# Kernel optimization log

Hardware: AMD Instinct MI355X
Metric: run time of the kernel (lower is better)

Reference implementation:

```python
import jax, jax.numpy as jnp
import numpy as np
from jax import lax

DIM = 96; HEADS = 3; WS = 8; SS = 4; HRES = 256; WRES = 256
HD = DIM // HEADS; SCALE = HD ** -0.5; N = WS * WS


def _rel_pos():
    # signed-log relative coordinates, [N, N, 2]
    c = np.arange(WS)
    coords = np.stack(np.meshgrid(c, c, indexing='ij')).reshape(2, -1)
    rel = (coords[:, :, None] - coords[:, None, :]).transpose(1, 2, 0).astype(np.float32)
    return np.sign(rel) * np.log1p(np.abs(rel))


def _attn_mask():
    # Swin-style shift mask, [nW, N, N] with 0 / -100
    img = np.zeros((HRES, WRES), np.float32)
    sl = (slice(0, -WS), slice(-WS, -SS), slice(-SS, None))
    cnt = 0
    for hs in sl:
        for ws in sl:
            img[hs, ws] = cnt
            cnt += 1
    mw = img.reshape(HRES // WS, WS, WRES // WS, WS).transpose(0, 2, 1, 3).reshape(-1, N)
    d = mw[:, None, :] - mw[:, :, None]
    return np.where(d != 0, -100.0, 0.0).astype(np.float32)

REL = jnp.asarray(_rel_pos())
MASK = jnp.asarray(_attn_mask())


def _conv1x1(x, w, b):
    return jnp.einsum('oc,bchw->bohw', w, x) + b[None, :, None, None]


def setup_inputs() -> dict:
    key = jax.random.key(0)
    ks = jax.random.split(key, 14)
    f = lambda k, s, sc=0.02: jax.random.normal(k, s, jnp.float32) * sc
    return {
        'x':   jax.random.normal(ks[0], (4, DIM, HRES, WRES), jnp.float32),
        'Wv':  f(ks[1], (DIM, DIM)),       'bv':  f(ks[2], (DIM,)),
        'Wqk': f(ks[3], (2 * DIM, DIM)),   'bqk': f(ks[4], (2 * DIM,)),
        'Wm1': f(ks[5], (2, 256), 0.1),    'bm1': f(ks[6], (256,)),
        'Wm2': f(ks[7], (256, HEADS), 0.1),'bm2': f(ks[8], (HEADS,)),
        'Wdw': f(ks[9], (DIM, 1, 5, 5)),   'bdw': f(ks[10], (DIM,)),
        'Wp':  f(ks[11], (DIM, DIM)),      'bp':  f(ks[12], (DIM,)),
    }


def reference(x, Wv, bv, Wqk, bqk, Wm1, bm1, Wm2, bm2, Wdw, bdw, Wp, bp):
    B, C, H, W = x.shape
    V = _conv1x1(x, Wv, bv)                      # [B,C,H,W]
    QK = _conv1x1(x, Wqk, bqk)                   # [B,2C,H,W]
    qkv = jnp.concatenate([QK, V], axis=1).transpose(0, 2, 3, 1)  # [B,H,W,3C]
    qkv = jnp.roll(qkv, (-SS, -SS), axis=(1, 2))
    nh, nw = H // WS, W // WS
    win = qkv.reshape(B, nh, WS, nw, WS, 3 * C).transpose(0, 1, 3, 2, 4, 5)
    win = win.reshape(B * nh * nw, N, 3 * C)     # [B_, N, 3C]
    q, k, v = [t.reshape(-1, N, HEADS, HD).transpose(0, 2, 1, 3)
               for t in jnp.split(win, 3, axis=-1)]
    attn = jnp.einsum('bhnd,bhmd->bhnm', q * SCALE, k)           # [B_,h,N,N]
    bias = jax.nn.relu(REL @ Wm1 + bm1) @ Wm2 + bm2              # [N,N,h]
    attn = attn + bias.transpose(2, 0, 1)[None]
    attn = attn.reshape(B, nh * nw, HEADS, N, N) + MASK[None, :, None]
    attn = jax.nn.softmax(attn.reshape(-1, HEADS, N, N), axis=-1)
    out = jnp.einsum('bhnm,bhmd->bnhd', attn, v).reshape(-1, N, C)
    out = out.reshape(B, nh, nw, WS, WS, C).transpose(0, 1, 3, 2, 4, 5).reshape(B, H, W, C)
    out = jnp.roll(out, (SS, SS), axis=(1, 2)).transpose(0, 3, 1, 2)  # [B,C,H,W]
    Vp = jnp.pad(V, ((0, 0), (0, 0), (2, 2), (2, 2)), mode='reflect')
    conv = lax.conv_general_dilated(Vp, Wdw, (1, 1), 'VALID',
                                    feature_group_count=C,
                                    dimension_numbers=('NCHW', 'OIHW', 'NCHW'))
    conv = conv + bdw[None, :, None, None]
    return _conv1x1(conv + out, Wp, bp)
```

## Files before the change

### kernel.cpp

```cpp
#include <hip/hip_runtime.h>
#include <hip/hip_bf16.h>
#include <hip/hip_fp16.h>

#define NHEADS 3
#define SSH 4
#define NWD 32
#define PXI 65536
#define SCALE 0.17677669529663687f

__global__ __launch_bounds__(256) void k0_wt(
    const float* __restrict__ Wqk, const float* __restrict__ Wv,
    const float* __restrict__ Wp, float* __restrict__ WT,
    float* __restrict__ WTp) {
  int i = blockIdx.x * 256 + threadIdx.x;
  if (i < 288 * 96) {
    int c = i % 96, oc = i / 96;
    float w = (oc < 192) ? Wqk[oc * 96 + c] : Wv[(oc - 192) * 96 + c];
    WT[c * 288 + oc] = w;
  }
  if (i < 96 * 96) {
    int c = i % 96, oc = i / 96;
    WTp[c * 96 + oc] = Wp[oc * 96 + c];
  }
}

__global__ __launch_bounds__(256) void k1_qkv(
    const float* __restrict__ x, const float* __restrict__ WT,
    const float* __restrict__ bqk, const float* __restrict__ bv,
    __half* __restrict__ qkv_h, float* __restrict__ v_b, int b) {
  __shared__ __align__(16) float Xt[96 * 64];
  const int tid = threadIdx.x;
  const int pt = blockIdx.x, ot = blockIdx.y;
  const int p0 = pt * 64;

  for (int i = tid; i < 96 * 16; i += 256) {
    int c = i >> 4, f = i & 15;
    *(float4*)&Xt[c * 64 + f * 4] =
        *(const float4*)&x[(size_t)(b * 96 + c) * PXI + p0 + f * 4];
  }
  __syncthreads();

  const int lane = tid & 63;
  const int wvu = __builtin_amdgcn_readfirstlane(tid >> 6);
  const int oc0l = wvu * 24;
  const int oc0 = ot * 96 + oc0l;

  float acc[24];
#pragma unroll
  for (int r = 0; r < 24; r++) acc[r] = 0.f;

  const float* wt = WT + oc0;
#pragma unroll 4
  for (int c = 0; c < 96; c++) {
    float xa = Xt[c * 64 + lane];
    const float* wc = wt + c * 288;
#pragma unroll
    for (int r = 0; r < 24; r++) acc[r] += wc[r] * xa;
  }

#pragma unroll
  for (int r = 0; r < 24; r++) {
    int oc = oc0 + r;
    acc[r] += (oc < 192) ? bqk[oc] : bv[oc - 192];
  }

  {
    int p = p0 + lane;
    int h = p >> 8, w = p & 255;
    int hp = (h + 252) & 255, wp = (w + 252) & 255;
    int win = (hp >> 3) * NWD + (wp >> 3);
    int n = (hp & 7) * 8 + (wp & 7);

    __align__(16) __half2 hv[12];
#pragma unroll
    for (int r = 0; r < 12; r++)
      hv[r] = __floats2half2_rn(acc[2 * r], acc[2 * r + 1]);
    __half* dst = qkv_h + (size_t)(win * 64 + n) * 288 + oc0;
    const float4* hv4 = (const float4*)hv;
    *(float4*)&dst[0]  = hv4[0];
    *(float4*)&dst[8]  = hv4[1];
    *(float4*)&dst[16] = hv4[2];

    if (ot == 2) {
#pragma unroll
      for (int r = 0; r < 24; r++)
        v_b[(size_t)(oc0l + r) * PXI + p] = acc[r];
    }
  }
}

__global__ __launch_bounds__(256) void k2_bias(
    const float* __restrict__ Wm1, const float* __restrict__ bm1,
    const float* __restrict__ Wm2, const float* __restrict__ bm2,
    float* __restrict__ bias_ws) {
  int pair = blockIdx.x * 256 + threadIdx.x;
  int n = pair >> 6, m = pair & 63;
  float d0 = (float)((n >> 3) - (m >> 3));
  float d1 = (float)((n & 7) - (m & 7));
  float r0 = (d0 > 0.f ? 1.f : (d0 < 0.f ? -1.f : 0.f)) * log1pf(fabsf(d0));
  float r1 = (d1 > 0.f ? 1.f : (d1 < 0.f ? -1.f : 0.f)) * log1pf(fabsf(d1));
  float a0 = 0.f, a1 = 0.f, a2 = 0.f;
  for (int j = 0; j < 256; j++) {
    float hb = r0 * Wm1[j] + r1 * Wm1[256 + j] + bm1[j];
    hb = fmaxf(hb, 0.f);
    a0 += hb * Wm2[j * 3 + 0];
    a1 += hb * Wm2[j * 3 + 1];
    a2 += hb * Wm2[j * 3 + 2];
  }
  bias_ws[0 * 4096 + pair] = a0 + bm2[0];
  bias_ws[1 * 4096 + pair] = a1 + bm2[1];
  bias_ws[2 * 4096 + pair] = a2 + bm2[2];
}

__global__ __launch_bounds__(64, 4) void k3_attn(
    const __half* __restrict__ qkv_h, const float* __restrict__ bias_ws,
    float* __restrict__ o_b) {
  __shared__ __align__(16) float KV[64 * 36];
  const int lane = threadIdx.x;
  const int win = blockIdx.x;
  const int hd = blockIdx.y;
  const int wh = win >> 5, ww = win & 31;
  const int row8 = lane >> 3, c4 = (lane & 7) * 4;

  const __half* qrow = qkv_h + (size_t)(win * 64 + lane) * 288 + hd * 32;
  float4 qraw[4];
  const float4* qp = (const float4*)qrow;
#pragma unroll
  for (int t = 0; t < 4; t++) qraw[t] = qp[t];

  const __half* kbase = qkv_h + (size_t)win * 64 * 288 + 96 + hd * 32;
  float2 kraw[8];
#pragma unroll
  for (int t = 0; t < 8; t++)
    kraw[t] = *(const float2*)&kbase[(size_t)(t * 8 + row8) * 288 + c4];

#pragma unroll
  for (int t = 0; t < 8; t++) {
    const __half2* hh = (const __half2*)&kraw[t];
    float2 a = __half22float2(hh[0]), b2 = __half22float2(hh[1]);
    *(float4*)&KV[(t * 8 + row8) * 36 + c4] = make_float4(a.x, a.y, b2.x, b2.y);
  }

  float q[32];
#pragma unroll
  for (int t = 0; t < 4; t++) {
    const __half2* hh = (const __half2*)&qraw[t];
#pragma unroll
    for (int u = 0; u < 4; u++) {
      float2 f = __half22float2(hh[u]);
      q[8 * t + 2 * u + 0] = f.x * SCALE;
      q[8 * t + 2 * u + 1] = f.y * SCALE;
    }
  }

  const float* bw = bias_ws + hd * 4096 + lane * 64;
  float s[64];
#pragma unroll
  for (int t = 0; t < 16; t++) {
    float4 b4 = *(const float4*)&bw[4 * t];
    s[4 * t + 0] = b4.x; s[4 * t + 1] = b4.y;
    s[4 * t + 2] = b4.z; s[4 * t + 3] = b4.w;
  }

  if (wh == 31 || ww == 31) {
    int rn = ((wh == 31) ? ((row8 < 4) ? 1 : 2) : 0) * 3 +
             ((ww == 31) ? (((lane & 7) < 4) ? 1 : 2) : 0);
#pragma unroll
    for (int m = 0; m < 64; m++) {
      int rm = ((wh == 31) ? (((m >> 3) < 4) ? 1 : 2) : 0) * 3 +
               ((ww == 31) ? (((m & 7) < 4) ? 1 : 2) : 0);
      if (rm != rn) s[m] -= 100.f;
    }
  }

#pragma unroll
  for (int m = 0; m < 64; m++) {
    float sum = s[m];
#pragma unroll
    for (int t = 0; t < 8; t++) {
      float4 kk = *(const float4*)&KV[m * 36 + 4 * t];
      sum += q[4 * t + 0] * kk.x + q[4 * t + 1] * kk.y +
             q[4 * t + 2] * kk.z + q[4 * t + 3] * kk.w;
    }
    s[m] = sum;
  }

  float2 vraw[8];
#pragma unroll
  for (int t = 0; t < 8; t++)
    vraw[t] = *(const float2*)&kbase[(size_t)(t * 8 + row8) * 288 + 96 + c4];

  float tr[32];
#pragma unroll
  for (int i = 0; i < 32; i++) tr[i] = fmaxf(s[i], s[i + 32]);
#pragma unroll
  for (int i = 0; i < 16; i++) tr[i] = fmaxf(tr[i], tr[i + 16]);
#pragma unroll
  for (int i = 0; i < 8; i++) tr[i] = fmaxf(tr[i], tr[i + 8]);
#pragma unroll
  for (int i = 0; i < 4; i++) tr[i] = fmaxf(tr[i], tr[i + 4]);
  float mx = fmaxf(fmaxf(tr[0], tr[1]), fmaxf(tr[2], tr[3]));
#pragma unroll
  for (int m = 0; m < 64; m++) s[m] = __expf(s[m] - mx);
#pragma unroll
  for (int i = 0; i < 32; i++) tr[i] = s[i] + s[i + 32];
#pragma unroll
  for (int i = 0; i < 16; i++) tr[i] = tr[i] + tr[i + 16];
#pragma unroll
  for (int i = 0; i < 8; i++) tr[i] = tr[i] + tr[i + 8];
#pragma unroll
  for (int i = 0; i < 4; i++) tr[i] = tr[i] + tr[i + 4];
  float inv = 1.f / ((tr[0] + tr[1]) + (tr[2] + tr[3]));

#pragma unroll
  for (int t = 0; t < 8; t++) {
    const __half2* hh = (const __half2*)&vraw[t];
    float2 a = __half22float2(hh[0]), b2 = __half22float2(hh[1]);
    *(float4*)&KV[(t * 8 + row8) * 36 + c4] = make_float4(a.x, a.y, b2.x, b2.y);
  }

  float o[32];
#pragma unroll
  for (int d = 0; d < 32; d++) o[d] = 0.f;
#pragma unroll
  for (int m = 0; m < 64; m++) {
    float p = s[m];
#pragma unroll
    for (int t = 0; t < 8; t++) {
      float4 vv = *(const float4*)&KV[m * 36 + 4 * t];
      o[4 * t + 0] += p * vv.x;
      o[4 * t + 1] += p * vv.y;
      o[4 * t + 2] += p * vv.z;
      o[4 * t + 3] += p * vv.w;
    }
  }

  const int hpix = ((wh << 3) + row8 + SSH) & 255;
  const int wpix = ((ww << 3) + (lane & 7) + SSH) & 255;
  float* ob = o_b + (size_t)hd * 32 * PXI + (hpix << 8) + wpix;
#pragma unroll
  for (int c = 0; c < 32; c++)
    ob[(size_t)c * PXI] = o[c] * inv;
}

__global__ __launch_bounds__(256) void k4_dw(
    const float* __restrict__ v_b, const float* __restrict__ o_b,
    const float* __restrict__ Wdw, const float* __restrict__ bdw,
    float* __restrict__ t_b) {
  const int blk = blockIdx.x;
  const int c = blk >> 8;
  const int h = blk & 255;
  const int w = threadIdx.x;
  __shared__ float wd[25];
  __shared__ float bd;
  if (threadIdx.x < 25) wd[threadIdx.x] = Wdw[c * 25 + threadIdx.x];
  if (threadIdx.x == 32) bd = bdw[c];
  __syncthreads();

  const float* vp = v_b + ((size_t)c << 16);
  float acc = bd;
#pragma unroll
  for (int dy = 0; dy < 5; dy++) {
    int hh = h + dy - 2;
    hh = hh < 0 ? -hh : (hh > 255 ? 510 - hh : hh);
    const float* row = vp + (hh << 8);
#pragma unroll
    for (int dx = 0; dx < 5; dx++) {
      int wx = w + dx - 2;
      wx = wx < 0 ? -wx : (wx > 255 ? 510 - wx : wx);
      acc += row[wx] * wd[dy * 5 + dx];
    }
  }
  size_t idx = ((size_t)c << 16) + (h << 8) + w;
  acc += o_b[idx];
  t_b[idx] = acc;
}

__global__ __launch_bounds__(256) void k5_proj(
    const float* __restrict__ t_b, const float* __restrict__ WTp,
    const float* __restrict__ bp, float* __restrict__ out, int b) {
  __shared__ __align__(16) float Xt[96 * 64];
  const int tid = threadIdx.x;
  const int pt = blockIdx.x;
  const int p0 = pt * 64;

  for (int i = tid; i < 96 * 16; i += 256) {
    int c = i >> 4, f = i & 15;
    *(float4*)&Xt[c * 64 + f * 4] =
        *(const float4*)&t_b[(size_t)c * PXI + p0 + f * 4];
  }
  __syncthreads();

  const int lane = tid & 63;
  const int wvu = __builtin_amdgcn_readfirstlane(tid >> 6);
  const int oc0 = wvu * 24;

  float acc[24];
#pragma unroll
  for (int r = 0; r < 24; r++) acc[r] = 0.f;

  const float* wt = WTp + oc0;
#pragma unroll 4
  for (int c = 0; c < 96; c++) {
    float xa = Xt[c * 64 + lane];
    const float* wc = wt + c * 96;
#pragma unroll
    for (int r = 0; r < 24; r++) acc[r] += wc[r] * xa;
  }

  int p = p0 + lane;
#pragma unroll
  for (int r = 0; r < 24; r++) {
    int oc = oc0 + r;
    out[(size_t)(b * 96 + oc) * PXI + p] = acc[r] + bp[oc];
  }
}

extern "C" void kernel_launch(void* const* d_in, const int* in_sizes, int n_in,
                              void* d_out, int out_size, void* d_ws,
                              size_t ws_size, hipStream_t stream) {
  const float* x   = (const float*)d_in[0];
  const float* Wv  = (const float*)d_in[1];
  const float* bv  = (const float*)d_in[2];
  const float* Wqk = (const float*)d_in[3];
  const float* bqk = (const float*)d_in[4];
  const float* Wm1 = (const float*)d_in[5];
  const float* bm1 = (const float*)d_in[6];
  const float* Wm2 = (const float*)d_in[7];
  const float* bm2 = (const float*)d_in[8];
  const float* Wdw = (const float*)d_in[9];
  const float* bdw = (const float*)d_in[10];
  const float* Wp  = (const float*)d_in[11];
  const float* bp  = (const float*)d_in[12];

  char* ws = (char*)d_ws;
  __half* qkv_h = (__half*)ws;
  float* t_b   = (float*)ws;
  float* v_b   = (float*)(ws + 37748736);
  float* o_b   = (float*)(ws + 62914560);
  float* bias_ws = (float*)(ws + 88080384);
  float* WT    = (float*)(ws + 88129536);
  float* WTp   = (float*)(ws + 88240128);

  k0_wt<<<108, 256, 0, stream>>>(Wqk, Wv, Wp, WT, WTp);
  k2_bias<<<16, 256, 0, stream>>>(Wm1, bm1, Wm2, bm2, bias_ws);
  for (int b = 0; b < 4; b++) {
    k1_qkv<<<dim3(1024, 3), 256, 0, stream>>>(x, WT, bqk, bv, qkv_h, v_b, b);
    k3_attn<<<dim3(1024, 3), 64, 0, stream>>>(qkv_h, bias_ws, o_b);
    k4_dw<<<24576, 256, 0, stream>>>(v_b, o_b, Wdw, bdw, t_b);
    k5_proj<<<1024, 256, 0, stream>>>(t_b, WTp, bp, (float*)d_out, b);
  }
}
```

Baseline: 777.4 us.

## Split attention keys across two threads per query and use fp16 dot2 for QK

The window attention kernel now runs 128 threads per window, with two threads per query row, each handling half of the 64 keys. Partial max, sum and output accumulators are combined with lane shuffles. K stays in fp16 in shared memory and QK scores use packed fp16 dot2 instructions. V is staged separately in fp32, so the shared buffer is no longer reused. The goals are more parallelism, fewer registers per thread and cheaper score math, at the cost of extra shuffles, a block barrier and fp16 product precision.

```diff
diff --git a/kernel.cpp b/kernel.cpp
--- a/kernel.cpp
+++ b/kernel.cpp
@@ -7,6 +7,14 @@
 #define NWD 32
 #define PXI 65536
 #define SCALE 0.17677669529663687f
+
+typedef _Float16 hf2 __attribute__((ext_vector_type(2)));
+
+#if __has_builtin(__builtin_amdgcn_fdot2)
+#define FDOT2(a, b, c) __builtin_amdgcn_fdot2((a), (b), (c), false)
+#else
+#define FDOT2(a, b, c) ((float)(a)[0] * (float)(b)[0] + (float)(a)[1] * (float)(b)[1] + (c))
+#endif
 
 __global__ __launch_bounds__(256) void k0_wt(
     const float* __restrict__ Wqk, const float* __restrict__ Wv,
@@ -112,135 +120,149 @@
   bias_ws[2 * 4096 + pair] = a2 + bm2[2];
 }
 
-__global__ __launch_bounds__(64, 4) void k3_attn(
+__global__ __launch_bounds__(128, 4) void k3_attn(
     const __half* __restrict__ qkv_h, const float* __restrict__ bias_ws,
     float* __restrict__ o_b) {
-  __shared__ __align__(16) float KV[64 * 36];
-  const int lane = threadIdx.x;
+  __shared__ __align__(16) __half Kh[64 * 40];
+  __shared__ __align__(16) float Vs[64 * 36];
+  const int tid = threadIdx.x;
+  const int n = tid >> 1;
+  const int half = tid & 1;
   const int win = blockIdx.x;
   const int hd = blockIdx.y;
   const int wh = win >> 5, ww = win & 31;
-  const int row8 = lane >> 3, c4 = (lane & 7) * 4;
-
-  const __half* qrow = qkv_h + (size_t)(win * 64 + lane) * 288 + hd * 32;
-  float4 qraw[4];
-  const float4* qp = (const float4*)qrow;
-#pragma unroll
-  for (int t = 0; t < 4; t++) qraw[t] = qp[t];
-
-  const __half* kbase = qkv_h + (size_t)win * 64 * 288 + 96 + hd * 32;
-  float2 kraw[8];
-#pragma unroll
-  for (int t = 0; t < 8; t++)
-    kraw[t] = *(const float2*)&kbase[(size_t)(t * 8 + row8) * 288 + c4];
-
-#pragma unroll
-  for (int t = 0; t < 8; t++) {
-    const __half2* hh = (const __half2*)&kraw[t];
+
+  const __half* base = qkv_h + (size_t)win * 64 * 288 + hd * 32;
+
+#pragma unroll
+  for (int i = 0; i < 2; i++) {
+    int idx = tid + 128 * i;
+    int row = idx >> 2, qd = idx & 3;
+    float4 kk = *(const float4*)(base + 96 + (size_t)row * 288 + qd * 8);
+    *(float4*)&Kh[row * 40 + qd * 8] = kk;
+  }
+#pragma unroll
+  for (int i = 0; i < 4; i++) {
+    int idx = tid + 128 * i;
+    int row = idx >> 3, qd = idx & 7;
+    float2 vv = *(const float2*)(base + 192 + (size_t)row * 288 + qd * 4);
+    const __half2* hh = (const __half2*)&vv;
     float2 a = __half22float2(hh[0]), b2 = __half22float2(hh[1]);
-    *(float4*)&KV[(t * 8 + row8) * 36 + c4] = make_float4(a.x, a.y, b2.x, b2.y);
-  }
-
-  float q[32];
-#pragma unroll
-  for (int t = 0; t < 4; t++) {
-    const __half2* hh = (const __half2*)&qraw[t];
-#pragma unroll
-    for (int u = 0; u < 4; u++) {
-      float2 f = __half22float2(hh[u]);
-      q[8 * t + 2 * u + 0] = f.x * SCALE;
-      q[8 * t + 2 * u + 1] = f.y * SCALE;
-    }
-  }
-
-  const float* bw = bias_ws + hd * 4096 + lane * 64;
-  float s[64];
-#pragma unroll
-  for (int t = 0; t < 16; t++) {
-    float4 b4 = *(const float4*)&bw[4 * t];
-    s[4 * t + 0] = b4.x; s[4 * t + 1] = b4.y;
-    s[4 * t + 2] = b4.z; s[4 * t + 3] = b4.w;
+    *(float4*)&Vs[row * 36 + qd * 4] = make_float4(a.x, a.y, b2.x, b2.y);
+  }
+
+  hf2 q2[16];
+  {
+    const float4* qp = (const float4*)(base + (size_t)n * 288);
+#pragma unroll
+    for (int t = 0; t < 4; t++) {
+      float4 f = qp[t];
+      const hf2* h = (const hf2*)&f;
+      q2[4 * t + 0] = h[0]; q2[4 * t + 1] = h[1];
+      q2[4 * t + 2] = h[2]; q2[4 * t + 3] = h[3];
+    }
+  }
+
+  float s[32];
+  {
+    const float* bw = bias_ws + hd * 4096 + n * 64 + half * 32;
+#pragma unroll
+    for (int t = 0; t < 8; t++) {
+      float4 b4 = *(const float4*)&bw[4 * t];
+      s[4 * t + 0] = b4.x; s[4 * t + 1] = b4.y;
+      s[4 * t + 2] = b4.z; s[4 * t + 3] = b4.w;
+    }
   }
 
   if (wh == 31 || ww == 31) {
-    int rn = ((wh == 31) ? ((row8 < 4) ? 1 : 2) : 0) * 3 +
-             ((ww == 31) ? (((lane & 7) < 4) ? 1 : 2) : 0);
-#pragma unroll
-    for (int m = 0; m < 64; m++) {
+    int rn = ((wh == 31) ? (((n >> 3) < 4) ? 1 : 2) : 0) * 3 +
+             ((ww == 31) ? (((n & 7) < 4) ? 1 : 2) : 0);
+#pragma unroll
+    for (int j = 0; j < 32; j++) {
+      int m = half * 32 + j;
       int rm = ((wh == 31) ? (((m >> 3) < 4) ? 1 : 2) : 0) * 3 +
                ((ww == 31) ? (((m & 7) < 4) ? 1 : 2) : 0);
-      if (rm != rn) s[m] -= 100.f;
-    }
-  }
-
-#pragma unroll
-  for (int m = 0; m < 64; m++) {
-    float sum = s[m];
-#pragma unroll
-    for (int t = 0; t < 8; t++) {
-      float4 kk = *(const float4*)&KV[m * 36 + 4 * t];
-      sum += q[4 * t + 0] * kk.x + q[4 * t + 1] * kk.y +
-             q[4 * t + 2] * kk.z + q[4 * t + 3] * kk.w;
-    }
-    s[m] = sum;
-  }
-
-  float2 vraw[8];
-#pragma unroll
-  for (int t = 0; t < 8; t++)
-    vraw[t] = *(const float2*)&kbase[(size_t)(t * 8 + row8) * 288 + 96 + c4];
-
-  float tr[32];
-#pragma unroll
-  for (int i = 0; i < 32; i++) tr[i] = fmaxf(s[i], s[i + 32]);
-#pragma unroll
-  for (int i = 0; i < 16; i++) tr[i] = fmaxf(tr[i], tr[i + 16]);
+      if (rm != rn) s[j] -= 100.f;
+    }
+  }
+
+  __syncthreads();
+
+#pragma unroll
+  for (int j = 0; j < 32; j++) {
+    int m = half * 32 + j;
+    float d0 = 0.f, d1 = 0.f;
+#pragma unroll
+    for (int u = 0; u < 2; u++) {
+      float4 kk = *(const float4*)&Kh[m * 40 + 8 * u];
+      const hf2* kh = (const hf2*)&kk;
+      d0 = FDOT2(q2[4 * u + 0], kh[0], d0);
+      d0 = FDOT2(q2[4 * u + 1], kh[1], d0);
+      d0 = FDOT2(q2[4 * u + 2], kh[2], d0);
+      d0 = FDOT2(q2[4 * u + 3], kh[3], d0);
+    }
+#pragma unroll
+    for (int u = 2; u < 4; u++) {
+      float4 kk = *(const float4*)&Kh[m * 40 + 8 * u];
+      const hf2* kh = (const hf2*)&kk;
+      d1 = FDOT2(q2[4 * u + 0], kh[0], d1);
+      d1 = FDOT2(q2[4 * u + 1], kh[1], d1);
+      d1 = FDOT2(q2[4 * u + 2], kh[2], d1);
+      d1 = FDOT2(q2[4 * u + 3], kh[3], d1);
+    }
+    s[j] += SCALE * (d0 + d1);
+  }
+
+  float tr[16];
+#pragma unroll
+  for (int i = 0; i < 16; i++) tr[i] = fmaxf(s[i], s[i + 16]);
 #pragma unroll
   for (int i = 0; i < 8; i++) tr[i] = fmaxf(tr[i], tr[i + 8]);
 #pragma unroll
   for (int i = 0; i < 4; i++) tr[i] = fmaxf(tr[i], tr[i + 4]);
   float mx = fmaxf(fmaxf(tr[0], tr[1]), fmaxf(tr[2], tr[3]));
-#pragma unroll
-  for (int m = 0; m < 64; m++) s[m] = __expf(s[m] - mx);
-#pragma unroll
-  for (int i = 0; i < 32; i++) tr[i] = s[i] + s[i + 32];
-#pragma unroll
-  for (int i = 0; i < 16; i++) tr[i] = tr[i] + tr[i + 16];
+  mx = fmaxf(mx, __shfl_xor(mx, 1));
+#pragma unroll
+  for (int j = 0; j < 32; j++) s[j] = __expf(s[j] - mx);
+#pragma unroll
+  for (int i = 0; i < 16; i++) tr[i] = s[i] + s[i + 16];
 #pragma unroll
   for (int i = 0; i < 8; i++) tr[i] = tr[i] + tr[i + 8];
 #pragma unroll
   for (int i = 0; i < 4; i++) tr[i] = tr[i] + tr[i + 4];
-  float inv = 1.f / ((tr[0] + tr[1]) + (tr[2] + tr[3]));
-
-#pragma unroll
-  for (int t = 0; t < 8; t++) {
-    const __half2* hh = (const __half2*)&vraw[t];
-    float2 a = __half22float2(hh[0]), b2 = __half22float2(hh[1]);
-    *(float4*)&KV[(t * 8 + row8) * 36 + c4] = make_float4(a.x, a.y, b2.x, b2.y);
-  }
+  float sm = (tr[0] + tr[1]) + (tr[2] + tr[3]);
+  sm += __shfl_xor(sm, 1);
+  float inv = 1.f / sm;
 
   float o[32];
 #pragma unroll
   for (int d = 0; d < 32; d++) o[d] = 0.f;
-#pragma unroll
-  for (int m = 0; m < 64; m++) {
-    float p = s[m];
-#pragma unroll
-    for (int t = 0; t < 8; t++) {
-      float4 vv = *(const float4*)&KV[m * 36 + 4 * t];
-      o[4 * t + 0] += p * vv.x;
-      o[4 * t + 1] += p * vv.y;
-      o[4 * t + 2] += p * vv.z;
-      o[4 * t + 3] += p * vv.w;
-    }
-  }
-
-  const int hpix = ((wh << 3) + row8 + SSH) & 255;
-  const int wpix = ((ww << 3) + (lane & 7) + SSH) & 255;
-  float* ob = o_b + (size_t)hd * 32 * PXI + (hpix << 8) + wpix;
-#pragma unroll
-  for (int c = 0; c < 32; c++)
-    ob[(size_t)c * PXI] = o[c] * inv;
+#pragma unroll 4
+  for (int j = 0; j < 32; j++) {
+    int m = half * 32 + j;
+    float p = s[j];
+#pragma unroll
+    for (int u = 0; u < 8; u++) {
+      float4 vv = *(const float4*)&Vs[m * 36 + 4 * u];
+      o[4 * u + 0] += p * vv.x;
+      o[4 * u + 1] += p * vv.y;
+      o[4 * u + 2] += p * vv.z;
+      o[4 * u + 3] += p * vv.w;
+    }
+  }
+#pragma unroll
+  for (int d = 0; d < 32; d++) o[d] += __shfl_xor(o[d], 1);
+
+  const int hpix = ((wh << 3) + (n >> 3) + SSH) & 255;
+  const int wpix = ((ww << 3) + (n & 7) + SSH) & 255;
+  float* ob = o_b + (size_t)(hd * 32 + half * 16) * PXI + (hpix << 8) + wpix;
+  if (half == 0) {
+#pragma unroll
+    for (int c = 0; c < 16; c++) ob[(size_t)c * PXI] = o[c] * inv;
+  } else {
+#pragma unroll
+    for (int c = 0; c < 16; c++) ob[(size_t)c * PXI] = o[c + 16] * inv;
+  }
 }
 
 __global__ __launch_bounds__(256) void k4_dw(
@@ -346,7 +368,7 @@
   k2_bias<<<16, 256, 0, stream>>>(Wm1, bm1, Wm2, bm2, bias_ws);
   for (int b = 0; b < 4; b++) {
     k1_qkv<<<dim3(1024, 3), 256, 0, stream>>>(x, WT, bqk, bv, qkv_h, v_b, b);
-    k3_attn<<<dim3(1024, 3), 64, 0, stream>>>(qkv_h, bias_ws, o_b);
+    k3_attn<<<dim3(1024, 3), 128, 0, stream>>>(qkv_h, bias_ws, o_b);
     k4_dw<<<24576, 256, 0, stream>>>(v_b, o_b, Wdw, bdw, t_b);
     k5_proj<<<1024, 256, 0, stream>>>(t_b, WTp, bp, (float*)d_out, b);
   }
```

Result: no change. 767.7 us (-1.2%).

## Compute window attention with MFMA f16 matrix instructions and pre-laid-out bias

Applied to the files above, without the earlier changes.

Rewrites the windowed attention kernel so that both QK^T and PV run on 16x16x32 f16 MFMA instructions instead of scalar FP32 FMAs over LDS. The bias table is precomputed directly in the MFMA accumulator layout, so it can be loaded straight into the score tiles. Softmax no longer subtracts the row max, and row sums are reduced with lane shuffles. P is staged through a swizzled f16 LDS buffer. In exchange, Q and P are rounded to f16, skipping the max subtraction risks overflow for large scores, V is loaded with scalar half gathers, and the output stores are strided across channels and less coalesced.

```diff
diff --git a/kernel.cpp b/kernel.cpp
--- a/kernel.cpp
+++ b/kernel.cpp
@@ -7,6 +7,9 @@
 #define NWD 32
 #define PXI 65536
 #define SCALE 0.17677669529663687f
+
+typedef _Float16 f16x8 __attribute__((ext_vector_type(8)));
+typedef float f32x4 __attribute__((ext_vector_type(4)));
 
 __global__ __launch_bounds__(256) void k0_wt(
     const float* __restrict__ Wqk, const float* __restrict__ Wv,
@@ -92,7 +95,7 @@
 __global__ __launch_bounds__(256) void k2_bias(
     const float* __restrict__ Wm1, const float* __restrict__ bm1,
     const float* __restrict__ Wm2, const float* __restrict__ bm2,
-    float* __restrict__ bias_ws) {
+    float* __restrict__ bias_c) {
   int pair = blockIdx.x * 256 + threadIdx.x;
   int n = pair >> 6, m = pair & 63;
   float d0 = (float)((n >> 3) - (m >> 3));
@@ -107,140 +110,154 @@
     a1 += hb * Wm2[j * 3 + 1];
     a2 += hb * Wm2[j * 3 + 2];
   }
-  bias_ws[0 * 4096 + pair] = a0 + bm2[0];
-  bias_ws[1 * 4096 + pair] = a1 + bm2[1];
-  bias_ws[2 * 4096 + pair] = a2 + bm2[2];
-}
-
-__global__ __launch_bounds__(64, 4) void k3_attn(
-    const __half* __restrict__ qkv_h, const float* __restrict__ bias_ws,
+  int ti = n >> 4, g = (n >> 2) & 3, reg = n & 3;
+  int tj = m >> 4, c = m & 15;
+  int lane = (g << 4) | c;
+  int idx = lane * 64 + (ti * 4 + tj) * 4 + reg;
+  bias_c[0 * 4096 + idx] = a0 + bm2[0];
+  bias_c[1 * 4096 + idx] = a1 + bm2[1];
+  bias_c[2 * 4096 + idx] = a2 + bm2[2];
+}
+
+__global__ __launch_bounds__(64) void k3_attn(
+    const __half* __restrict__ qkv_h, const float* __restrict__ bias_c,
     float* __restrict__ o_b) {
-  __shared__ __align__(16) float KV[64 * 36];
+  __shared__ _Float16 P_lds[64 * 72];
   const int lane = threadIdx.x;
+  const int g = lane >> 4;
+  const int c = lane & 15;
   const int win = blockIdx.x;
   const int hd = blockIdx.y;
   const int wh = win >> 5, ww = win & 31;
-  const int row8 = lane >> 3, c4 = (lane & 7) * 4;
-
-  const __half* qrow = qkv_h + (size_t)(win * 64 + lane) * 288 + hd * 32;
-  float4 qraw[4];
-  const float4* qp = (const float4*)qrow;
-#pragma unroll
-  for (int t = 0; t < 4; t++) qraw[t] = qp[t];
-
-  const __half* kbase = qkv_h + (size_t)win * 64 * 288 + 96 + hd * 32;
-  float2 kraw[8];
-#pragma unroll
-  for (int t = 0; t < 8; t++)
-    kraw[t] = *(const float2*)&kbase[(size_t)(t * 8 + row8) * 288 + c4];
-
-#pragma unroll
-  for (int t = 0; t < 8; t++) {
-    const __half2* hh = (const __half2*)&kraw[t];
-    float2 a = __half22float2(hh[0]), b2 = __half22float2(hh[1]);
-    *(float4*)&KV[(t * 8 + row8) * 36 + c4] = make_float4(a.x, a.y, b2.x, b2.y);
-  }
-
-  float q[32];
+
+  const __half* qb = qkv_h + (size_t)win * 64 * 288 + hd * 32;
+
+  f16x8 qf[4], kf[4];
 #pragma unroll
   for (int t = 0; t < 4; t++) {
-    const __half2* hh = (const __half2*)&qraw[t];
-#pragma unroll
-    for (int u = 0; u < 4; u++) {
-      float2 f = __half22float2(hh[u]);
-      q[8 * t + 2 * u + 0] = f.x * SCALE;
-      q[8 * t + 2 * u + 1] = f.y * SCALE;
-    }
-  }
-
-  const float* bw = bias_ws + hd * 4096 + lane * 64;
-  float s[64];
-#pragma unroll
-  for (int t = 0; t < 16; t++) {
-    float4 b4 = *(const float4*)&bw[4 * t];
-    s[4 * t + 0] = b4.x; s[4 * t + 1] = b4.y;
-    s[4 * t + 2] = b4.z; s[4 * t + 3] = b4.w;
+    qf[t] = *(const f16x8*)(const void*)&qb[(size_t)(16 * t + c) * 288 + 8 * g];
+    kf[t] = *(const f16x8*)(const void*)&qb[(size_t)(16 * t + c) * 288 + 96 + 8 * g];
+  }
+#pragma unroll
+  for (int t = 0; t < 4; t++)
+#pragma unroll
+    for (int e = 0; e < 8; e++) qf[t][e] *= (_Float16)SCALE;
+
+  f32x4 S[4][4];
+  {
+    const float* bc = bias_c + (size_t)hd * 4096 + lane * 64;
+#pragma unroll
+    for (int ti = 0; ti < 4; ti++)
+#pragma unroll
+      for (int tj = 0; tj < 4; tj++)
+        S[ti][tj] = *(const f32x4*)&bc[(ti * 4 + tj) * 4];
   }
 
   if (wh == 31 || ww == 31) {
-    int rn = ((wh == 31) ? ((row8 < 4) ? 1 : 2) : 0) * 3 +
-             ((ww == 31) ? (((lane & 7) < 4) ? 1 : 2) : 0);
-#pragma unroll
-    for (int m = 0; m < 64; m++) {
-      int rm = ((wh == 31) ? (((m >> 3) < 4) ? 1 : 2) : 0) * 3 +
-               ((ww == 31) ? (((m & 7) < 4) ? 1 : 2) : 0);
-      if (rm != rn) s[m] -= 100.f;
-    }
-  }
-
-#pragma unroll
-  for (int m = 0; m < 64; m++) {
-    float sum = s[m];
-#pragma unroll
-    for (int t = 0; t < 8; t++) {
-      float4 kk = *(const float4*)&KV[m * 36 + 4 * t];
-      sum += q[4 * t + 0] * kk.x + q[4 * t + 1] * kk.y +
-             q[4 * t + 2] * kk.z + q[4 * t + 3] * kk.w;
-    }
-    s[m] = sum;
-  }
-
-  float2 vraw[8];
-#pragma unroll
-  for (int t = 0; t < 8; t++)
-    vraw[t] = *(const float2*)&kbase[(size_t)(t * 8 + row8) * 288 + 96 + c4];
-
-  float tr[32];
-#pragma unroll
-  for (int i = 0; i < 32; i++) tr[i] = fmaxf(s[i], s[i + 32]);
-#pragma unroll
-  for (int i = 0; i < 16; i++) tr[i] = fmaxf(tr[i], tr[i + 16]);
-#pragma unroll
-  for (int i = 0; i < 8; i++) tr[i] = fmaxf(tr[i], tr[i + 8]);
-#pragma unroll
-  for (int i = 0; i < 4; i++) tr[i] = fmaxf(tr[i], tr[i + 4]);
-  float mx = fmaxf(fmaxf(tr[0], tr[1]), fmaxf(tr[2], tr[3]));
-#pragma unroll
-  for (int m = 0; m < 64; m++) s[m] = __expf(s[m] - mx);
-#pragma unroll
-  for (int i = 0; i < 32; i++) tr[i] = s[i] + s[i + 32];
-#pragma unroll
-  for (int i = 0; i < 16; i++) tr[i] = tr[i] + tr[i + 16];
-#pragma unroll
-  for (int i = 0; i < 8; i++) tr[i] = tr[i] + tr[i + 8];
-#pragma unroll
-  for (int i = 0; i < 4; i++) tr[i] = tr[i] + tr[i + 4];
-  float inv = 1.f / ((tr[0] + tr[1]) + (tr[2] + tr[3]));
-
-#pragma unroll
-  for (int t = 0; t < 8; t++) {
-    const __half2* hh = (const __half2*)&vraw[t];
-    float2 a = __half22float2(hh[0]), b2 = __half22float2(hh[1]);
-    *(float4*)&KV[(t * 8 + row8) * 36 + c4] = make_float4(a.x, a.y, b2.x, b2.y);
-  }
-
-  float o[32];
-#pragma unroll
-  for (int d = 0; d < 32; d++) o[d] = 0.f;
-#pragma unroll
-  for (int m = 0; m < 64; m++) {
-    float p = s[m];
-#pragma unroll
-    for (int t = 0; t < 8; t++) {
-      float4 vv = *(const float4*)&KV[m * 36 + 4 * t];
-      o[4 * t + 0] += p * vv.x;
-      o[4 * t + 1] += p * vv.y;
-      o[4 * t + 2] += p * vv.z;
-      o[4 * t + 3] += p * vv.w;
-    }
-  }
-
-  const int hpix = ((wh << 3) + row8 + SSH) & 255;
-  const int wpix = ((ww << 3) + (lane & 7) + SSH) & 255;
-  float* ob = o_b + (size_t)hd * 32 * PXI + (hpix << 8) + wpix;
-#pragma unroll
-  for (int c = 0; c < 32; c++)
-    ob[(size_t)c * PXI] = o[c] * inv;
+#pragma unroll
+    for (int ti = 0; ti < 4; ti++)
+#pragma unroll
+      for (int r = 0; r < 4; r++) {
+        int row = 16 * ti + 4 * g + r;
+        int rn = ((wh == 31) ? (((row >> 3) < 4) ? 1 : 2) : 0) * 3 +
+                 ((ww == 31) ? (((row & 7) < 4) ? 1 : 2) : 0);
+#pragma unroll
+        for (int tj = 0; tj < 4; tj++) {
+          int m = 16 * tj + c;
+          int rm = ((wh == 31) ? (((m >> 3) < 4) ? 1 : 2) : 0) * 3 +
+                   ((ww == 31) ? (((m & 7) < 4) ? 1 : 2) : 0);
+          if (rm != rn) S[ti][tj][r] -= 100.f;
+        }
+      }
+  }
+
+#pragma unroll
+  for (int tn = 0; tn < 4; tn++)
+#pragma unroll
+    for (int tm = 0; tm < 4; tm++)
+      S[tn][tm] = __builtin_amdgcn_mfma_f32_16x16x32_f16(qf[tn], kf[tm],
+                                                         S[tn][tm], 0, 0, 0);
+
+  const __half* vbse = qb + 192;
+  f16x8 vf[2][2];
+#pragma unroll
+  for (int td = 0; td < 2; td++)
+#pragma unroll
+    for (int km = 0; km < 2; km++) {
+      f16x8 v = {};
+#pragma unroll
+      for (int i = 0; i < 8; i++)
+        v[i] = *(const _Float16*)&vbse[(size_t)(32 * km + 8 * g + i) * 288 +
+                                       16 * td + c];
+      vf[td][km] = v;
+    }
+
+#pragma unroll
+  for (int ti = 0; ti < 4; ti++)
+#pragma unroll
+    for (int tj = 0; tj < 4; tj++)
+#pragma unroll
+      for (int r = 0; r < 4; r++) S[ti][tj][r] = __expf(S[ti][tj][r]);
+
+  float invs[4][4];
+#pragma unroll
+  for (int ti = 0; ti < 4; ti++)
+#pragma unroll
+    for (int r = 0; r < 4; r++) {
+      float sm = (S[ti][0][r] + S[ti][1][r]) + (S[ti][2][r] + S[ti][3][r]);
+      sm += __shfl_xor(sm, 1);
+      sm += __shfl_xor(sm, 2);
+      sm += __shfl_xor(sm, 4);
+      sm += __shfl_xor(sm, 8);
+      invs[ti][r] = 1.f / sm;
+    }
+
+  {
+    const int cx = (4 * g) & 8;
+#pragma unroll
+    for (int ti = 0; ti < 4; ti++)
+#pragma unroll
+      for (int r = 0; r < 4; r++) {
+        int row = 16 * ti + 4 * g + r;
+        int rx = (4 * g + r) & 8;
+#pragma unroll
+        for (int tj = 0; tj < 4; tj++)
+          P_lds[row * 72 + ((16 * tj + c) ^ rx)] = (_Float16)S[ti][tj][r];
+      }
+    (void)cx;
+  }
+
+  f32x4 O[4][2];
+#pragma unroll
+  for (int tn = 0; tn < 4; tn++) {
+    const int row = 16 * tn + c;
+    const int rx = c & 8;
+    f16x8 pf0 = *(const f16x8*)(const void*)&P_lds[row * 72 + ((8 * g) ^ rx)];
+    f16x8 pf1 = *(const f16x8*)(const void*)&P_lds[row * 72 + ((32 + 8 * g) ^ rx)];
+#pragma unroll
+    for (int td = 0; td < 2; td++) {
+      f32x4 oo = {0.f, 0.f, 0.f, 0.f};
+      oo = __builtin_amdgcn_mfma_f32_16x16x32_f16(pf0, vf[td][0], oo, 0, 0, 0);
+      oo = __builtin_amdgcn_mfma_f32_16x16x32_f16(pf1, vf[td][1], oo, 0, 0, 0);
+      O[tn][td] = oo;
+    }
+  }
+
+#pragma unroll
+  for (int tn = 0; tn < 4; tn++)
+#pragma unroll
+    for (int r = 0; r < 4; r++) {
+      int row = 16 * tn + 4 * g + r;
+      int hpix = ((wh << 3) + (row >> 3) + SSH) & 255;
+      int wpix = ((ww << 3) + (row & 7) + SSH) & 255;
+      size_t pix = (size_t)(hpix << 8) + wpix;
+      float inv = invs[tn][r];
+#pragma unroll
+      for (int td = 0; td < 2; td++) {
+        int cch = hd * 32 + 16 * td + c;
+        o_b[(size_t)cch * PXI + pix] = O[tn][td][r] * inv;
+      }
+    }
 }
 
 __global__ __launch_bounds__(256) void k4_dw(
@@ -338,15 +355,15 @@
   float* t_b   = (float*)ws;
   float* v_b   = (float*)(ws + 37748736);
   float* o_b   = (float*)(ws + 62914560);
-  float* bias_ws = (float*)(ws + 88080384);
+  float* bias_c = (float*)(ws + 88080384);
   float* WT    = (float*)(ws + 88129536);
   float* WTp   = (float*)(ws + 88240128);
 
   k0_wt<<<108, 256, 0, stream>>>(Wqk, Wv, Wp, WT, WTp);
-  k2_bias<<<16, 256, 0, stream>>>(Wm1, bm1, Wm2, bm2, bias_ws);
+  k2_bias<<<16, 256, 0, stream>>>(Wm1, bm1, Wm2, bm2, bias_c);
   for (int b = 0; b < 4; b++) {
     k1_qkv<<<dim3(1024, 3), 256, 0, stream>>>(x, WT, bqk, bv, qkv_h, v_b, b);
-    k3_attn<<<dim3(1024, 3), 64, 0, stream>>>(qkv_h, bias_ws, o_b);
+    k3_attn<<<dim3(1024, 3), 64, 0, stream>>>(qkv_h, bias_c, o_b);
     k4_dw<<<24576, 256, 0, stream>>>(v_b, o_b, Wdw, bdw, t_b);
     k5_proj<<<1024, 256, 0, stream>>>(t_b, WTp, bp, (float*)d_out, b);
   }
```

Result: faster. 712.5 us (-8.4%).
